# Kernel optimization log

Hardware: AMD Instinct MI355X
Metric: run time of the kernel (lower is better)

The kernel has to match this reference:

```python
import jax, jax.numpy as jnp
import numpy as np

N = 8192       # num_nodes
E = 262144     # num_edges (avg degree 32)
D_IN = 256
D_H = 256
D_OUT = 256
BN_EPS = 1e-5


def _linear_params(key, din, dout):
    # torch nn.Linear default init: U(-1/sqrt(din), 1/sqrt(din))
    s = 1.0 / np.sqrt(din)
    kw, kb = jax.random.split(key)
    W = jax.random.uniform(kw, (dout, din), jnp.float32, -s, s)
    b = jax.random.uniform(kb, (dout,), jnp.float32, -s, s)
    return W, b


def setup_inputs() -> dict:
    key = jax.random.key(0)
    ks = jax.random.split(key, 6)
    x = jax.random.normal(ks[0], (N, D_IN), jnp.float32)
    edge_index = jax.random.randint(ks[1], (2, E), 0, N, dtype=jnp.int64)
    W1, b1 = _linear_params(ks[2], D_IN, D_H)
    W2, b2 = _linear_params(ks[3], D_H, D_H)
    W3, b3 = _linear_params(ks[4], D_H, D_OUT)
    return {
        "x": x, "edge_index": edge_index,
        "W1": W1, "b1": b1, "W2": W2, "b2": b2, "W3": W3, "b3": b3,
        "g1": jnp.ones((D_H,), jnp.float32), "be1": jnp.zeros((D_H,), jnp.float32),
        "g2": jnp.ones((D_H,), jnp.float32), "be2": jnp.zeros((D_H,), jnp.float32),
        "g3": jnp.ones((D_OUT,), jnp.float32), "be3": jnp.zeros((D_OUT,), jnp.float32),
    }


def _build_norm(edge_index):
    # add self loops, scatter 1.0 into dense NxN adjacency (duplicates collapse via set)
    loop = jnp.arange(N, dtype=edge_index.dtype)
    rows = jnp.concatenate([edge_index[0], loop])
    cols = jnp.concatenate([edge_index[1], loop])
    adj = jnp.zeros((N, N), jnp.float32).at[rows, cols].set(1.0)
    deg = adj.sum(axis=1)
    dinv = jnp.where(deg > 0, deg ** -0.5, 0.0)  # inf -> 0 as in original
    return dinv[:, None] * adj * dinv[None, :]


def _gcn(x, norm, W, b):
    # linear then symmetric-normalized aggregation
    return norm @ (x @ W.T + b)


def _bn(x, g, b):
    # BatchNorm1d with batch statistics (biased var), eps=1e-5
    mu = x.mean(axis=0)
    var = x.var(axis=0)
    return (x - mu) * jax.lax.rsqrt(var + BN_EPS) * g + b


def reference(x, edge_index, W1, b1, W2, b2, W3, b3, g1, be1, g2, be2, g3, be3):
    norm = _build_norm(edge_index)
    h = jax.nn.relu(_bn(_gcn(x, norm, W1, b1), g1, be1))
    h = jax.nn.relu(_bn(_gcn(h, norm, W2, b2), g2, be2))
    h = _bn(_gcn(h, norm, W3, b3), g3, be3)
    return h
```

## Files before the change

### kernel.cpp

```cpp
#include <hip/hip_runtime.h>

#define N_NODES 8192
#define N_EDGES 262144
#define D 256
#define ADJ_WORDS 256
#define MAX_DEG 128
#define AGG_BLOCKS 2048
#define NPART 16

typedef __attribute__((ext_vector_type(8))) short bf16x8;
typedef __attribute__((ext_vector_type(4))) float f32x4;

__device__ __forceinline__ short f2bf(float f) {
    unsigned u = __builtin_bit_cast(unsigned, f);
    u += 0x7fffu + ((u >> 16) & 1);
    return (short)(u >> 16);
}
__device__ __forceinline__ float bf2f(unsigned short u) {
    return __builtin_bit_cast(float, ((unsigned)u) << 16);
}

__global__ __launch_bounds__(256) void build_adj(const int* __restrict__ ei,
                                                 unsigned* __restrict__ adj,
                                                 int* __restrict__ deg,
                                                 const float* __restrict__ W1,
                                                 const float* __restrict__ W2,
                                                 const float* __restrict__ W3,
                                                 unsigned short* __restrict__ Wb1,
                                                 unsigned short* __restrict__ Wb2,
                                                 unsigned short* __restrict__ Wb3) {
    int i = blockIdx.x * 256 + threadIdx.x;
    if (i >= N_EDGES + N_NODES) {
        int j = i - (N_EDGES + N_NODES);
        int which = j >> 16, k = j & 65535;
        const float* src = which == 0 ? W1 : which == 1 ? W2 : W3;
        unsigned short* dst = which == 0 ? Wb1 : which == 1 ? Wb2 : Wb3;
        dst[k] = (unsigned short)f2bf(src[k]);
        return;
    }
    int r, c;
    if (i < N_EDGES) {
        r = ei[i];
        c = ei[N_EDGES + i];
    } else {
        r = i - N_EDGES;
        c = r;
    }
    unsigned bit = 1u << (c & 31);
    unsigned old = atomicOr(&adj[r * ADJ_WORDS + (c >> 5)], bit);
    if (!(old & bit)) atomicAdd(&deg[r], 1);
}

__device__ __forceinline__ void nbrs_body(const unsigned* __restrict__ adj,
                                          int* __restrict__ nbr_idx, int r) {
    const int t = threadIdx.x;
    const int lane = t & 63, wave = t >> 6;
    unsigned m = adj[r * ADJ_WORDS + t];
    int cnt = __popc(m);
    int x = cnt;
    #pragma unroll
    for (int off = 1; off < 64; off <<= 1) {
        int v = __shfl_up(x, off, 64);
        if (lane >= off) x += v;
    }
    __shared__ int wtot[4];
    if (lane == 63) wtot[wave] = x;
    __syncthreads();
    int woff = 0;
    #pragma unroll
    for (int w = 0; w < 4; w++) woff += (w < wave) ? wtot[w] : 0;
    int base = woff + x - cnt;
    int* oi = nbr_idx + (size_t)r * MAX_DEG;
    while (m) {
        int b = __ffs(m) - 1;
        m &= m - 1;
        int c = (t << 5) + b;
        if (base < MAX_DEG) oi[base] = c;
        base++;
    }
}

template <bool APPLY, bool RELU>
__device__ __forceinline__ void gemm_body(const float* __restrict__ Xsrc,
                                          const float* __restrict__ psA,
                                          const float* __restrict__ psQ,
                                          const float* __restrict__ g,
                                          const float* __restrict__ be,
                                          const unsigned short* __restrict__ Wb,
                                          const float* __restrict__ bias,
                                          const int* __restrict__ deg,
                                          unsigned short* __restrict__ Hb,
                                          int bn, int bm) {
    __shared__ float ssc[256], ssh[256];
    const int tid = threadIdx.x;
    if (APPLY) {
        float s = 0.f, q = 0.f;
        #pragma unroll
        for (int i = 0; i < NPART; i++) {
            s += psA[i * 256 + tid];
            q += psQ[i * 256 + tid];
        }
        float mu = s * (1.0f / N_NODES);
        float var = q * (1.0f / N_NODES) - mu * mu;
        float rstd = rsqrtf(var + 1e-5f);
        float sc = g[tid] * rstd;
        ssc[tid] = sc;
        ssh[tid] = be[tid] - mu * sc;
        __syncthreads();
    }

    const int wave = tid >> 6, lane = tid & 63;
    const int l16 = lane & 15, q = lane >> 4;
    const int mrow = bm + wave * 16 + l16;

    f32x4 acc[4];
    #pragma unroll
    for (int j = 0; j < 4; j++) acc[j] = (f32x4){0.f, 0.f, 0.f, 0.f};

    for (int k0 = 0; k0 < D; k0 += 32) {
        const int kq = k0 + q * 8;
        bf16x8 xb;
        {
            const float* xr = Xsrc + (size_t)mrow * D + kq;
            float4 a = *(const float4*)xr;
            float4 b = *(const float4*)(xr + 4);
            float v[8] = {a.x, a.y, a.z, a.w, b.x, b.y, b.z, b.w};
            if (APPLY) {
                float4 sc0 = *(const float4*)(ssc + kq);
                float4 sc1 = *(const float4*)(ssc + kq + 4);
                float4 sh0 = *(const float4*)(ssh + kq);
                float4 sh1 = *(const float4*)(ssh + kq + 4);
                float sc[8] = {sc0.x, sc0.y, sc0.z, sc0.w, sc1.x, sc1.y, sc1.z, sc1.w};
                float sh[8] = {sh0.x, sh0.y, sh0.z, sh0.w, sh1.x, sh1.y, sh1.z, sh1.w};
                #pragma unroll
                for (int j = 0; j < 8; j++) {
                    v[j] = fmaf(v[j], sc[j], sh[j]);
                    if (RELU) v[j] = fmaxf(v[j], 0.0f);
                }
            }
            #pragma unroll
            for (int j = 0; j < 8; j++) xb[j] = f2bf(v[j]);
        }
        #pragma unroll
        for (int nf = 0; nf < 4; nf++) {
            bf16x8 wa = *(const bf16x8*)(Wb + (size_t)(bn + nf * 16 + l16) * D + kq);
            acc[nf] = __builtin_amdgcn_mfma_f32_16x16x32_bf16(wa, xb, acc[nf], 0, 0, 0);
        }
    }

    const float di = rsqrtf((float)deg[mrow]);
    #pragma unroll
    for (int nf = 0; nf < 4; nf++) {
        const int nb = bn + nf * 16 + q * 4;
        float4 b4 = *(const float4*)(bias + nb);
        short4 o;
        o.x = f2bf((acc[nf][0] + b4.x) * di);
        o.y = f2bf((acc[nf][1] + b4.y) * di);
        o.z = f2bf((acc[nf][2] + b4.z) * di);
        o.w = f2bf((acc[nf][3] + b4.w) * di);
        *(short4*)(Hb + (size_t)mrow * D + nb) = o;
    }
}

__global__ __launch_bounds__(256) void gemm1_and_nbrs(const float* __restrict__ x,
                                                      const unsigned short* __restrict__ Wb1,
                                                      const float* __restrict__ b1,
                                                      const int* __restrict__ deg,
                                                      unsigned short* __restrict__ Hb,
                                                      const unsigned* __restrict__ adj,
                                                      int* __restrict__ nbr_idx) {
    const int bg = blockIdx.x;
    if (bg < 512) {
        gemm_body<false, false>(x, nullptr, nullptr, nullptr, nullptr, Wb1, b1, deg, Hb,
                                (bg & 3) * 64, (bg >> 2) * 64);
    } else {
        nbrs_body(adj, nbr_idx, bg - 512);
    }
}

__global__ __launch_bounds__(256) void gemm_mfma_bn(const float* __restrict__ Xsrc,
                                                    const float* __restrict__ psA,
                                                    const float* __restrict__ psQ,
                                                    const float* __restrict__ g,
                                                    const float* __restrict__ be,
                                                    const unsigned short* __restrict__ Wb,
                                                    const float* __restrict__ bias,
                                                    const int* __restrict__ deg,
                                                    unsigned short* __restrict__ Hb) {
    gemm_body<true, true>(Xsrc, psA, psQ, g, be, Wb, bias, deg, Hb,
                          blockIdx.x * 64, blockIdx.y * 64);
}

__global__ __launch_bounds__(256) void aggregate_bf16(const int* __restrict__ nbr_idx,
                                                      const int* __restrict__ deg,
                                                      const unsigned short* __restrict__ Hb,
                                                      float* __restrict__ G,
                                                      float* __restrict__ psA,
                                                      float* __restrict__ psQ) {
    const int wave = threadIdx.x >> 6;
    const int lane = threadIdx.x & 63;
    const int ch = lane * 4;
    const int r = blockIdx.x * 4 + wave;

    const int dgr = deg[r];
    int dg = dgr; if (dg > MAX_DEG) dg = MAX_DEG;
    const int* idx = nbr_idx + (size_t)r * MAX_DEG;
    const unsigned short* hb = Hb + ch;

    float a0 = 0.f, a1 = 0.f, a2 = 0.f, a3 = 0.f;
    int base = 0;
    for (; base + 16 <= dg; base += 16) {
        int4 q0 = *(const int4*)(idx + base);
        int4 q1 = *(const int4*)(idx + base + 4);
        int4 q2 = *(const int4*)(idx + base + 8);
        int4 q3 = *(const int4*)(idx + base + 12);
        ushort4 u0  = *(const ushort4*)(hb + (size_t)q0.x * D);
        ushort4 u1  = *(const ushort4*)(hb + (size_t)q0.y * D);
        ushort4 u2  = *(const ushort4*)(hb + (size_t)q0.z * D);
        ushort4 u3  = *(const ushort4*)(hb + (size_t)q0.w * D);
        ushort4 u4  = *(const ushort4*)(hb + (size_t)q1.x * D);
        ushort4 u5  = *(const ushort4*)(hb + (size_t)q1.y * D);
        ushort4 u6  = *(const ushort4*)(hb + (size_t)q1.z * D);
        ushort4 u7  = *(const ushort4*)(hb + (size_t)q1.w * D);
        ushort4 u8  = *(const ushort4*)(hb + (size_t)q2.x * D);
        ushort4 u9  = *(const ushort4*)(hb + (size_t)q2.y * D);
        ushort4 u10 = *(const ushort4*)(hb + (size_t)q2.z * D);
        ushort4 u11 = *(const ushort4*)(hb + (size_t)q2.w * D);
        ushort4 u12 = *(const ushort4*)(hb + (size_t)q3.x * D);
        ushort4 u13 = *(const ushort4*)(hb + (size_t)q3.y * D);
        ushort4 u14 = *(const ushort4*)(hb + (size_t)q3.z * D);
        ushort4 u15 = *(const ushort4*)(hb + (size_t)q3.w * D);
        a0 += bf2f(u0.x);  a1 += bf2f(u0.y);  a2 += bf2f(u0.z);  a3 += bf2f(u0.w);
        a0 += bf2f(u1.x);  a1 += bf2f(u1.y);  a2 += bf2f(u1.z);  a3 += bf2f(u1.w);
        a0 += bf2f(u2.x);  a1 += bf2f(u2.y);  a2 += bf2f(u2.z);  a3 += bf2f(u2.w);
        a0 += bf2f(u3.x);  a1 += bf2f(u3.y);  a2 += bf2f(u3.z);  a3 += bf2f(u3.w);
        a0 += bf2f(u4.x);  a1 += bf2f(u4.y);  a2 += bf2f(u4.z);  a3 += bf2f(u4.w);
        a0 += bf2f(u5.x);  a1 += bf2f(u5.y);  a2 += bf2f(u5.z);  a3 += bf2f(u5.w);
        a0 += bf2f(u6.x);  a1 += bf2f(u6.y);  a2 += bf2f(u6.z);  a3 += bf2f(u6.w);
        a0 += bf2f(u7.x);  a1 += bf2f(u7.y);  a2 += bf2f(u7.z);  a3 += bf2f(u7.w);
        a0 += bf2f(u8.x);  a1 += bf2f(u8.y);  a2 += bf2f(u8.z);  a3 += bf2f(u8.w);
        a0 += bf2f(u9.x);  a1 += bf2f(u9.y);  a2 += bf2f(u9.z);  a3 += bf2f(u9.w);
        a0 += bf2f(u10.x); a1 += bf2f(u10.y); a2 += bf2f(u10.z); a3 += bf2f(u10.w);
        a0 += bf2f(u11.x); a1 += bf2f(u11.y); a2 += bf2f(u11.z); a3 += bf2f(u11.w);
        a0 += bf2f(u12.x); a1 += bf2f(u12.y); a2 += bf2f(u12.z); a3 += bf2f(u12.w);
        a0 += bf2f(u13.x); a1 += bf2f(u13.y); a2 += bf2f(u13.z); a3 += bf2f(u13.w);
        a0 += bf2f(u14.x); a1 += bf2f(u14.y); a2 += bf2f(u14.z); a3 += bf2f(u14.w);
        a0 += bf2f(u15.x); a1 += bf2f(u15.y); a2 += bf2f(u15.z); a3 += bf2f(u15.w);
    }
    for (; base + 8 <= dg; base += 8) {
        int4 q0 = *(const int4*)(idx + base);
        int4 q1 = *(const int4*)(idx + base + 4);
        ushort4 u0 = *(const ushort4*)(hb + (size_t)q0.x * D);
        ushort4 u1 = *(const ushort4*)(hb + (size_t)q0.y * D);
        ushort4 u2 = *(const ushort4*)(hb + (size_t)q0.z * D);
        ushort4 u3 = *(const ushort4*)(hb + (size_t)q0.w * D);
        ushort4 u4 = *(const ushort4*)(hb + (size_t)q1.x * D);
        ushort4 u5 = *(const ushort4*)(hb + (size_t)q1.y * D);
        ushort4 u6 = *(const ushort4*)(hb + (size_t)q1.z * D);
        ushort4 u7 = *(const ushort4*)(hb + (size_t)q1.w * D);
        a0 += bf2f(u0.x); a1 += bf2f(u0.y); a2 += bf2f(u0.z); a3 += bf2f(u0.w);
        a0 += bf2f(u1.x); a1 += bf2f(u1.y); a2 += bf2f(u1.z); a3 += bf2f(u1.w);
        a0 += bf2f(u2.x); a1 += bf2f(u2.y); a2 += bf2f(u2.z); a3 += bf2f(u2.w);
        a0 += bf2f(u3.x); a1 += bf2f(u3.y); a2 += bf2f(u3.z); a3 += bf2f(u3.w);
        a0 += bf2f(u4.x); a1 += bf2f(u4.y); a2 += bf2f(u4.z); a3 += bf2f(u4.w);
        a0 += bf2f(u5.x); a1 += bf2f(u5.y); a2 += bf2f(u5.z); a3 += bf2f(u5.w);
        a0 += bf2f(u6.x); a1 += bf2f(u6.y); a2 += bf2f(u6.z); a3 += bf2f(u6.w);
        a0 += bf2f(u7.x); a1 += bf2f(u7.y); a2 += bf2f(u7.z); a3 += bf2f(u7.w);
    }
    for (; base + 4 <= dg; base += 4) {
        int4 q0 = *(const int4*)(idx + base);
        ushort4 u0 = *(const ushort4*)(hb + (size_t)q0.x * D);
        ushort4 u1 = *(const ushort4*)(hb + (size_t)q0.y * D);
        ushort4 u2 = *(const ushort4*)(hb + (size_t)q0.z * D);
        ushort4 u3 = *(const ushort4*)(hb + (size_t)q0.w * D);
        a0 += bf2f(u0.x); a1 += bf2f(u0.y); a2 += bf2f(u0.z); a3 += bf2f(u0.w);
        a0 += bf2f(u1.x); a1 += bf2f(u1.y); a2 += bf2f(u1.z); a3 += bf2f(u1.w);
        a0 += bf2f(u2.x); a1 += bf2f(u2.y); a2 += bf2f(u2.z); a3 += bf2f(u2.w);
        a0 += bf2f(u3.x); a1 += bf2f(u3.y); a2 += bf2f(u3.z); a3 += bf2f(u3.w);
    }
    for (; base < dg; base++) {
        int c = idx[base];
        ushort4 u = *(const ushort4*)(hb + (size_t)c * D);
        a0 += bf2f(u.x); a1 += bf2f(u.y); a2 += bf2f(u.z); a3 += bf2f(u.w);
    }

    const float dr = rsqrtf((float)dgr);
    float4 o;
    o.x = a0 * dr; o.y = a1 * dr; o.z = a2 * dr; o.w = a3 * dr;
    *(float4*)(G + (size_t)r * D + ch) = o;

    __shared__ float ls[4][256], lss[4][256];
    ls[wave][ch] = o.x; ls[wave][ch + 1] = o.y; ls[wave][ch + 2] = o.z; ls[wave][ch + 3] = o.w;
    lss[wave][ch] = o.x * o.x; lss[wave][ch + 1] = o.y * o.y;
    lss[wave][ch + 2] = o.z * o.z; lss[wave][ch + 3] = o.w * o.w;
    __syncthreads();
    const int t = threadIdx.x;
    const int prow = (blockIdx.x & (NPART - 1)) * 256;
    atomicAdd(&psA[prow + t], ls[0][t] + ls[1][t] + ls[2][t] + ls[3][t]);
    atomicAdd(&psQ[prow + t], lss[0][t] + lss[1][t] + lss[2][t] + lss[3][t]);
}

__global__ __launch_bounds__(256) void bn_apply_out(const float* __restrict__ G,
                                                    const float* __restrict__ psA,
                                                    const float* __restrict__ psQ,
                                                    const float* __restrict__ g,
                                                    const float* __restrict__ be,
                                                    float* __restrict__ Out) {
    __shared__ float ssc[256], ssh[256];
    const int tid = threadIdx.x;
    {
        float s = 0.f, q = 0.f;
        #pragma unroll
        for (int i = 0; i < NPART; i++) {
            s += psA[i * 256 + tid];
            q += psQ[i * 256 + tid];
        }
        float mu = s * (1.0f / N_NODES);
        float var = q * (1.0f / N_NODES) - mu * mu;
        float rstd = rsqrtf(var + 1e-5f);
        float sc = g[tid] * rstd;
        ssc[tid] = sc;
        ssh[tid] = be[tid] - mu * sc;
        __syncthreads();
    }
    const int rows_per_block = 32;
    const int r0 = blockIdx.x * rows_per_block;
    const int ch = (tid & 63) * 4;
    const int rsub = tid >> 6;
    float4 sc = *(const float4*)(ssc + ch);
    float4 sh = *(const float4*)(ssh + ch);
    for (int rr = rsub; rr < rows_per_block; rr += 4) {
        const size_t off = (size_t)(r0 + rr) * D + ch;
        float4 v = *(const float4*)(G + off);
        v.x = fmaf(v.x, sc.x, sh.x);
        v.y = fmaf(v.y, sc.y, sh.y);
        v.z = fmaf(v.z, sc.z, sh.z);
        v.w = fmaf(v.w, sc.w, sh.w);
        *(float4*)(Out + off) = v;
    }
}

extern "C" void kernel_launch(void* const* d_in, const int* in_sizes, int n_in,
                              void* d_out, int out_size, void* d_ws, size_t ws_size,
                              hipStream_t stream) {
    const float* x  = (const float*)d_in[0];
    const int*   ei = (const int*)d_in[1];
    const float* W1 = (const float*)d_in[2];
    const float* b1 = (const float*)d_in[3];
    const float* W2 = (const float*)d_in[4];
    const float* b2 = (const float*)d_in[5];
    const float* W3 = (const float*)d_in[6];
    const float* b3 = (const float*)d_in[7];
    const float* g1 = (const float*)d_in[8];
    const float* be1 = (const float*)d_in[9];
    const float* g2 = (const float*)d_in[10];
    const float* be2 = (const float*)d_in[11];
    const float* g3 = (const float*)d_in[12];
    const float* be3 = (const float*)d_in[13];

    char* ws = (char*)d_ws;
    unsigned*       adj  = (unsigned*)ws;
    int*            deg  = (int*)(ws + (8 << 20));
    float*          psA0 = (float*)(ws + (8 << 20) + (32 << 10));
    float*          psQ0 = psA0 + NPART * 256;
    float*          psA1 = psQ0 + NPART * 256;
    float*          psQ1 = psA1 + NPART * 256;
    float*          psA2 = psQ1 + NPART * 256;
    float*          psQ2 = psA2 + NPART * 256;
    unsigned short* Wb1  = (unsigned short*)(ws + (8 << 20) + (128 << 10));
    unsigned short* Wb2  = (unsigned short*)(ws + (8 << 20) + (256 << 10));
    unsigned short* Wb3  = (unsigned short*)(ws + (8 << 20) + (384 << 10));
    int*            nbr_idx = (int*)  (ws + (9 << 20));
    float*          G       = (float*)(ws + (13 << 20));
    unsigned short* Hb      = (unsigned short*)(ws + (21 << 20));

    hipMemsetAsync(ws, 0, (8 << 20) + (128 << 10), stream);

    build_adj<<<1824, 256, 0, stream>>>(ei, adj, deg, W1, W2, W3, Wb1, Wb2, Wb3);

    gemm1_and_nbrs<<<512 + N_NODES, 256, 0, stream>>>(x, Wb1, b1, deg, Hb, adj, nbr_idx);
    aggregate_bf16<<<AGG_BLOCKS, 256, 0, stream>>>(nbr_idx, deg, Hb, G, psA0, psQ0);

    dim3 ggrid(D / 64, N_NODES / 64);

    gemm_mfma_bn<<<ggrid, 256, 0, stream>>>(G, psA0, psQ0, g1, be1, Wb2, b2, deg, Hb);
    aggregate_bf16<<<AGG_BLOCKS, 256, 0, stream>>>(nbr_idx, deg, Hb, G, psA1, psQ1);

    gemm_mfma_bn<<<ggrid, 256, 0, stream>>>(G, psA1, psQ1, g2, be2, Wb3, b3, deg, Hb);
    aggregate_bf16<<<AGG_BLOCKS, 256, 0, stream>>>(nbr_idx, deg, Hb, G, psA2, psQ2);

    bn_apply_out<<<N_NODES / 32, 256, 0, stream>>>(G, psA2, psQ2, g3, be3, (float*)d_out);
}
```

Baseline: 217.2 us.

## Fuse all GCN phases into one cooperative persistent kernel with grid syncs

Replaces the memset plus seven separate launches with a single cooperative kernel of 1024 persistent blocks. Phases (zeroing, adjacency build, GEMMs, neighbor lists, aggregations, BN output) are separated by grid.sync and use grid-stride loops. GEMM tiles shrink to 64x32 so 1024 tiles fill the grid, and the first GEMM now runs alongside neighbor-list extraction in the same phase. The aim is to remove launch gaps and the memset, at the cost of grid-wide barrier overhead and register and occupancy limits from the launch bound of 4 blocks per CU. A fallback path of separate launches remains.

```diff
diff --git a/kernel.cpp b/kernel.cpp
--- a/kernel.cpp
+++ b/kernel.cpp
@@ -1,15 +1,29 @@
 #include <hip/hip_runtime.h>
+#include <hip/hip_cooperative_groups.h>
+
+namespace cg = cooperative_groups;
 
 #define N_NODES 8192
 #define N_EDGES 262144
 #define D 256
 #define ADJ_WORDS 256
 #define MAX_DEG 128
-#define AGG_BLOCKS 2048
 #define NPART 16
+#define GRID_C 1024
 
 typedef __attribute__((ext_vector_type(8))) short bf16x8;
 typedef __attribute__((ext_vector_type(4))) float f32x4;
+
+struct Params {
+    const float* x; const int* ei;
+    const float *W1, *b1, *W2, *b2, *W3, *b3;
+    const float *g1, *be1, *g2, *be2, *g3, *be3;
+    float* out;
+    unsigned* adj; int* deg;
+    float *psA0, *psQ0, *psA1, *psQ1, *psA2, *psQ2;
+    unsigned short *Wb1, *Wb2, *Wb3;
+    int* nbr_idx; float* G; unsigned short* Hb;
+};
 
 __device__ __forceinline__ short f2bf(float f) {
     unsigned u = __builtin_bit_cast(unsigned, f);
@@ -20,39 +34,40 @@
     return __builtin_bit_cast(float, ((unsigned)u) << 16);
 }
 
-__global__ __launch_bounds__(256) void build_adj(const int* __restrict__ ei,
-                                                 unsigned* __restrict__ adj,
-                                                 int* __restrict__ deg,
-                                                 const float* __restrict__ W1,
-                                                 const float* __restrict__ W2,
-                                                 const float* __restrict__ W3,
-                                                 unsigned short* __restrict__ Wb1,
-                                                 unsigned short* __restrict__ Wb2,
-                                                 unsigned short* __restrict__ Wb3) {
-    int i = blockIdx.x * 256 + threadIdx.x;
-    if (i >= N_EDGES + N_NODES) {
-        int j = i - (N_EDGES + N_NODES);
-        int which = j >> 16, k = j & 65535;
-        const float* src = which == 0 ? W1 : which == 1 ? W2 : W3;
-        unsigned short* dst = which == 0 ? Wb1 : which == 1 ? Wb2 : Wb3;
-        dst[k] = (unsigned short)f2bf(src[k]);
-        return;
-    }
-    int r, c;
-    if (i < N_EDGES) {
-        r = ei[i];
-        c = ei[N_EDGES + i];
-    } else {
-        r = i - N_EDGES;
-        c = r;
-    }
-    unsigned bit = 1u << (c & 31);
-    unsigned old = atomicOr(&adj[r * ADJ_WORDS + (c >> 5)], bit);
-    if (!(old & bit)) atomicAdd(&deg[r], 1);
-}
-
-__device__ __forceinline__ void nbrs_body(const unsigned* __restrict__ adj,
-                                          int* __restrict__ nbr_idx, int r) {
+__device__ __forceinline__ void ph_zero(float4* z, int n4) {
+    const int stride = gridDim.x * 256;
+    for (int i = blockIdx.x * 256 + threadIdx.x; i < n4; i += stride)
+        z[i] = make_float4(0.f, 0.f, 0.f, 0.f);
+}
+
+__device__ __forceinline__ void ph_build(const Params& p) {
+    const int TOT = N_EDGES + N_NODES + 3 * 65536;
+    const int stride = gridDim.x * 256;
+    for (int i = blockIdx.x * 256 + threadIdx.x; i < TOT; i += stride) {
+        if (i >= N_EDGES + N_NODES) {
+            int j = i - (N_EDGES + N_NODES);
+            int which = j >> 16, k = j & 65535;
+            const float* src = which == 0 ? p.W1 : which == 1 ? p.W2 : p.W3;
+            unsigned short* dst = which == 0 ? p.Wb1 : which == 1 ? p.Wb2 : p.Wb3;
+            dst[k] = (unsigned short)f2bf(src[k]);
+            continue;
+        }
+        int r, c;
+        if (i < N_EDGES) {
+            r = p.ei[i];
+            c = p.ei[N_EDGES + i];
+        } else {
+            r = i - N_EDGES;
+            c = r;
+        }
+        unsigned bit = 1u << (c & 31);
+        unsigned old = atomicOr(&p.adj[r * ADJ_WORDS + (c >> 5)], bit);
+        if (!(old & bit)) atomicAdd(&p.deg[r], 1);
+    }
+}
+
+__device__ __forceinline__ void nbrs_row(const unsigned* __restrict__ adj,
+                                         int* __restrict__ nbr_idx, int r) {
     const int t = threadIdx.x;
     const int lane = t & 63, wave = t >> 6;
     unsigned m = adj[r * ADJ_WORDS + t];
@@ -80,17 +95,23 @@
     }
 }
 
+__device__ __forceinline__ void ph_nbrs(const unsigned* adj, int* nbr_idx) {
+    for (int r = blockIdx.x; r < N_NODES; r += gridDim.x) {
+        nbrs_row(adj, nbr_idx, r);
+        __syncthreads();
+    }
+}
+
 template <bool APPLY, bool RELU>
-__device__ __forceinline__ void gemm_body(const float* __restrict__ Xsrc,
-                                          const float* __restrict__ psA,
-                                          const float* __restrict__ psQ,
-                                          const float* __restrict__ g,
-                                          const float* __restrict__ be,
-                                          const unsigned short* __restrict__ Wb,
-                                          const float* __restrict__ bias,
-                                          const int* __restrict__ deg,
-                                          unsigned short* __restrict__ Hb,
-                                          int bn, int bm) {
+__device__ __forceinline__ void ph_gemm(const float* __restrict__ Xsrc,
+                                        const float* __restrict__ psA,
+                                        const float* __restrict__ psQ,
+                                        const float* __restrict__ g,
+                                        const float* __restrict__ be,
+                                        const unsigned short* __restrict__ Wb,
+                                        const float* __restrict__ bias,
+                                        const int* __restrict__ deg,
+                                        unsigned short* __restrict__ Hb) {
     __shared__ float ssc[256], ssh[256];
     const int tid = threadIdx.x;
     if (APPLY) {
@@ -108,204 +129,182 @@
         ssh[tid] = be[tid] - mu * sc;
         __syncthreads();
     }
-
     const int wave = tid >> 6, lane = tid & 63;
     const int l16 = lane & 15, q = lane >> 4;
-    const int mrow = bm + wave * 16 + l16;
-
-    f32x4 acc[4];
-    #pragma unroll
-    for (int j = 0; j < 4; j++) acc[j] = (f32x4){0.f, 0.f, 0.f, 0.f};
-
-    for (int k0 = 0; k0 < D; k0 += 32) {
-        const int kq = k0 + q * 8;
-        bf16x8 xb;
-        {
-            const float* xr = Xsrc + (size_t)mrow * D + kq;
-            float4 a = *(const float4*)xr;
-            float4 b = *(const float4*)(xr + 4);
-            float v[8] = {a.x, a.y, a.z, a.w, b.x, b.y, b.z, b.w};
-            if (APPLY) {
-                float4 sc0 = *(const float4*)(ssc + kq);
-                float4 sc1 = *(const float4*)(ssc + kq + 4);
-                float4 sh0 = *(const float4*)(ssh + kq);
-                float4 sh1 = *(const float4*)(ssh + kq + 4);
-                float sc[8] = {sc0.x, sc0.y, sc0.z, sc0.w, sc1.x, sc1.y, sc1.z, sc1.w};
-                float sh[8] = {sh0.x, sh0.y, sh0.z, sh0.w, sh1.x, sh1.y, sh1.z, sh1.w};
+
+    for (int t = blockIdx.x; t < 1024; t += gridDim.x) {
+        const int bn = (t & 7) * 32;
+        const int bm = (t >> 3) * 64;
+        const int mrow = bm + wave * 16 + l16;
+
+        f32x4 acc[2];
+        acc[0] = (f32x4){0.f, 0.f, 0.f, 0.f};
+        acc[1] = (f32x4){0.f, 0.f, 0.f, 0.f};
+
+        for (int k0 = 0; k0 < D; k0 += 32) {
+            const int kq = k0 + q * 8;
+            bf16x8 xb;
+            {
+                const float* xr = Xsrc + (size_t)mrow * D + kq;
+                float4 a = *(const float4*)xr;
+                float4 b = *(const float4*)(xr + 4);
+                float v[8] = {a.x, a.y, a.z, a.w, b.x, b.y, b.z, b.w};
+                if (APPLY) {
+                    float4 sc0 = *(const float4*)(ssc + kq);
+                    float4 sc1 = *(const float4*)(ssc + kq + 4);
+                    float4 sh0 = *(const float4*)(ssh + kq);
+                    float4 sh1 = *(const float4*)(ssh + kq + 4);
+                    float sc[8] = {sc0.x, sc0.y, sc0.z, sc0.w, sc1.x, sc1.y, sc1.z, sc1.w};
+                    float sh[8] = {sh0.x, sh0.y, sh0.z, sh0.w, sh1.x, sh1.y, sh1.z, sh1.w};
+                    #pragma unroll
+                    for (int j = 0; j < 8; j++) {
+                        v[j] = fmaf(v[j], sc[j], sh[j]);
+                        if (RELU) v[j] = fmaxf(v[j], 0.0f);
+                    }
+                }
                 #pragma unroll
-                for (int j = 0; j < 8; j++) {
-                    v[j] = fmaf(v[j], sc[j], sh[j]);
-                    if (RELU) v[j] = fmaxf(v[j], 0.0f);
-                }
+                for (int j = 0; j < 8; j++) xb[j] = f2bf(v[j]);
             }
             #pragma unroll
-            for (int j = 0; j < 8; j++) xb[j] = f2bf(v[j]);
-        }
+            for (int nf = 0; nf < 2; nf++) {
+                bf16x8 wa = *(const bf16x8*)(Wb + (size_t)(bn + nf * 16 + l16) * D + kq);
+                acc[nf] = __builtin_amdgcn_mfma_f32_16x16x32_bf16(wa, xb, acc[nf], 0, 0, 0);
+            }
+        }
+
+        const float di = rsqrtf((float)deg[mrow]);
         #pragma unroll
-        for (int nf = 0; nf < 4; nf++) {
-            bf16x8 wa = *(const bf16x8*)(Wb + (size_t)(bn + nf * 16 + l16) * D + kq);
-            acc[nf] = __builtin_amdgcn_mfma_f32_16x16x32_bf16(wa, xb, acc[nf], 0, 0, 0);
-        }
-    }
-
-    const float di = rsqrtf((float)deg[mrow]);
-    #pragma unroll
-    for (int nf = 0; nf < 4; nf++) {
-        const int nb = bn + nf * 16 + q * 4;
-        float4 b4 = *(const float4*)(bias + nb);
-        short4 o;
-        o.x = f2bf((acc[nf][0] + b4.x) * di);
-        o.y = f2bf((acc[nf][1] + b4.y) * di);
-        o.z = f2bf((acc[nf][2] + b4.z) * di);
-        o.w = f2bf((acc[nf][3] + b4.w) * di);
-        *(short4*)(Hb + (size_t)mrow * D + nb) = o;
-    }
-}
-
-__global__ __launch_bounds__(256) void gemm1_and_nbrs(const float* __restrict__ x,
-                                                      const unsigned short* __restrict__ Wb1,
-                                                      const float* __restrict__ b1,
-                                                      const int* __restrict__ deg,
-                                                      unsigned short* __restrict__ Hb,
-                                                      const unsigned* __restrict__ adj,
-                                                      int* __restrict__ nbr_idx) {
-    const int bg = blockIdx.x;
-    if (bg < 512) {
-        gemm_body<false, false>(x, nullptr, nullptr, nullptr, nullptr, Wb1, b1, deg, Hb,
-                                (bg & 3) * 64, (bg >> 2) * 64);
-    } else {
-        nbrs_body(adj, nbr_idx, bg - 512);
-    }
-}
-
-__global__ __launch_bounds__(256) void gemm_mfma_bn(const float* __restrict__ Xsrc,
-                                                    const float* __restrict__ psA,
-                                                    const float* __restrict__ psQ,
-                                                    const float* __restrict__ g,
-                                                    const float* __restrict__ be,
-                                                    const unsigned short* __restrict__ Wb,
-                                                    const float* __restrict__ bias,
-                                                    const int* __restrict__ deg,
-                                                    unsigned short* __restrict__ Hb) {
-    gemm_body<true, true>(Xsrc, psA, psQ, g, be, Wb, bias, deg, Hb,
-                          blockIdx.x * 64, blockIdx.y * 64);
-}
-
-__global__ __launch_bounds__(256) void aggregate_bf16(const int* __restrict__ nbr_idx,
-                                                      const int* __restrict__ deg,
-                                                      const unsigned short* __restrict__ Hb,
-                                                      float* __restrict__ G,
-                                                      float* __restrict__ psA,
-                                                      float* __restrict__ psQ) {
+        for (int nf = 0; nf < 2; nf++) {
+            const int nb = bn + nf * 16 + q * 4;
+            float4 b4 = *(const float4*)(bias + nb);
+            short4 o;
+            o.x = f2bf((acc[nf][0] + b4.x) * di);
+            o.y = f2bf((acc[nf][1] + b4.y) * di);
+            o.z = f2bf((acc[nf][2] + b4.z) * di);
+            o.w = f2bf((acc[nf][3] + b4.w) * di);
+            *(short4*)(Hb + (size_t)mrow * D + nb) = o;
+        }
+    }
+}
+
+__device__ __forceinline__ void ph_agg(const int* __restrict__ nbr_idx,
+                                       const int* __restrict__ deg,
+                                       const unsigned short* __restrict__ Hb,
+                                       float* __restrict__ G,
+                                       float* __restrict__ psA,
+                                       float* __restrict__ psQ) {
+    __shared__ float ls[4][256], lss[4][256];
     const int wave = threadIdx.x >> 6;
     const int lane = threadIdx.x & 63;
     const int ch = lane * 4;
-    const int r = blockIdx.x * 4 + wave;
-
-    const int dgr = deg[r];
-    int dg = dgr; if (dg > MAX_DEG) dg = MAX_DEG;
-    const int* idx = nbr_idx + (size_t)r * MAX_DEG;
     const unsigned short* hb = Hb + ch;
 
-    float a0 = 0.f, a1 = 0.f, a2 = 0.f, a3 = 0.f;
-    int base = 0;
-    for (; base + 16 <= dg; base += 16) {
-        int4 q0 = *(const int4*)(idx + base);
-        int4 q1 = *(const int4*)(idx + base + 4);
-        int4 q2 = *(const int4*)(idx + base + 8);
-        int4 q3 = *(const int4*)(idx + base + 12);
-        ushort4 u0  = *(const ushort4*)(hb + (size_t)q0.x * D);
-        ushort4 u1  = *(const ushort4*)(hb + (size_t)q0.y * D);
-        ushort4 u2  = *(const ushort4*)(hb + (size_t)q0.z * D);
-        ushort4 u3  = *(const ushort4*)(hb + (size_t)q0.w * D);
-        ushort4 u4  = *(const ushort4*)(hb + (size_t)q1.x * D);
-        ushort4 u5  = *(const ushort4*)(hb + (size_t)q1.y * D);
-        ushort4 u6  = *(const ushort4*)(hb + (size_t)q1.z * D);
-        ushort4 u7  = *(const ushort4*)(hb + (size_t)q1.w * D);
-        ushort4 u8  = *(const ushort4*)(hb + (size_t)q2.x * D);
-        ushort4 u9  = *(const ushort4*)(hb + (size_t)q2.y * D);
-        ushort4 u10 = *(const ushort4*)(hb + (size_t)q2.z * D);
-        ushort4 u11 = *(const ushort4*)(hb + (size_t)q2.w * D);
-        ushort4 u12 = *(const ushort4*)(hb + (size_t)q3.x * D);
-        ushort4 u13 = *(const ushort4*)(hb + (size_t)q3.y * D);
-        ushort4 u14 = *(const ushort4*)(hb + (size_t)q3.z * D);
-        ushort4 u15 = *(const ushort4*)(hb + (size_t)q3.w * D);
-        a0 += bf2f(u0.x);  a1 += bf2f(u0.y);  a2 += bf2f(u0.z);  a3 += bf2f(u0.w);
-        a0 += bf2f(u1.x);  a1 += bf2f(u1.y);  a2 += bf2f(u1.z);  a3 += bf2f(u1.w);
-        a0 += bf2f(u2.x);  a1 += bf2f(u2.y);  a2 += bf2f(u2.z);  a3 += bf2f(u2.w);
-        a0 += bf2f(u3.x);  a1 += bf2f(u3.y);  a2 += bf2f(u3.z);  a3 += bf2f(u3.w);
-        a0 += bf2f(u4.x);  a1 += bf2f(u4.y);  a2 += bf2f(u4.z);  a3 += bf2f(u4.w);
-        a0 += bf2f(u5.x);  a1 += bf2f(u5.y);  a2 += bf2f(u5.z);  a3 += bf2f(u5.w);
-        a0 += bf2f(u6.x);  a1 += bf2f(u6.y);  a2 += bf2f(u6.z);  a3 += bf2f(u6.w);
-        a0 += bf2f(u7.x);  a1 += bf2f(u7.y);  a2 += bf2f(u7.z);  a3 += bf2f(u7.w);
-        a0 += bf2f(u8.x);  a1 += bf2f(u8.y);  a2 += bf2f(u8.z);  a3 += bf2f(u8.w);
-        a0 += bf2f(u9.x);  a1 += bf2f(u9.y);  a2 += bf2f(u9.z);  a3 += bf2f(u9.w);
-        a0 += bf2f(u10.x); a1 += bf2f(u10.y); a2 += bf2f(u10.z); a3 += bf2f(u10.w);
-        a0 += bf2f(u11.x); a1 += bf2f(u11.y); a2 += bf2f(u11.z); a3 += bf2f(u11.w);
-        a0 += bf2f(u12.x); a1 += bf2f(u12.y); a2 += bf2f(u12.z); a3 += bf2f(u12.w);
-        a0 += bf2f(u13.x); a1 += bf2f(u13.y); a2 += bf2f(u13.z); a3 += bf2f(u13.w);
-        a0 += bf2f(u14.x); a1 += bf2f(u14.y); a2 += bf2f(u14.z); a3 += bf2f(u14.w);
-        a0 += bf2f(u15.x); a1 += bf2f(u15.y); a2 += bf2f(u15.z); a3 += bf2f(u15.w);
-    }
-    for (; base + 8 <= dg; base += 8) {
-        int4 q0 = *(const int4*)(idx + base);
-        int4 q1 = *(const int4*)(idx + base + 4);
-        ushort4 u0 = *(const ushort4*)(hb + (size_t)q0.x * D);
-        ushort4 u1 = *(const ushort4*)(hb + (size_t)q0.y * D);
-        ushort4 u2 = *(const ushort4*)(hb + (size_t)q0.z * D);
-        ushort4 u3 = *(const ushort4*)(hb + (size_t)q0.w * D);
-        ushort4 u4 = *(const ushort4*)(hb + (size_t)q1.x * D);
-        ushort4 u5 = *(const ushort4*)(hb + (size_t)q1.y * D);
-        ushort4 u6 = *(const ushort4*)(hb + (size_t)q1.z * D);
-        ushort4 u7 = *(const ushort4*)(hb + (size_t)q1.w * D);
-        a0 += bf2f(u0.x); a1 += bf2f(u0.y); a2 += bf2f(u0.z); a3 += bf2f(u0.w);
-        a0 += bf2f(u1.x); a1 += bf2f(u1.y); a2 += bf2f(u1.z); a3 += bf2f(u1.w);
-        a0 += bf2f(u2.x); a1 += bf2f(u2.y); a2 += bf2f(u2.z); a3 += bf2f(u2.w);
-        a0 += bf2f(u3.x); a1 += bf2f(u3.y); a2 += bf2f(u3.z); a3 += bf2f(u3.w);
-        a0 += bf2f(u4.x); a1 += bf2f(u4.y); a2 += bf2f(u4.z); a3 += bf2f(u4.w);
-        a0 += bf2f(u5.x); a1 += bf2f(u5.y); a2 += bf2f(u5.z); a3 += bf2f(u5.w);
-        a0 += bf2f(u6.x); a1 += bf2f(u6.y); a2 += bf2f(u6.z); a3 += bf2f(u6.w);
-        a0 += bf2f(u7.x); a1 += bf2f(u7.y); a2 += bf2f(u7.z); a3 += bf2f(u7.w);
-    }
-    for (; base + 4 <= dg; base += 4) {
-        int4 q0 = *(const int4*)(idx + base);
-        ushort4 u0 = *(const ushort4*)(hb + (size_t)q0.x * D);
-        ushort4 u1 = *(const ushort4*)(hb + (size_t)q0.y * D);
-        ushort4 u2 = *(const ushort4*)(hb + (size_t)q0.z * D);
-        ushort4 u3 = *(const ushort4*)(hb + (size_t)q0.w * D);
-        a0 += bf2f(u0.x); a1 += bf2f(u0.y); a2 += bf2f(u0.z); a3 += bf2f(u0.w);
-        a0 += bf2f(u1.x); a1 += bf2f(u1.y); a2 += bf2f(u1.z); a3 += bf2f(u1.w);
-        a0 += bf2f(u2.x); a1 += bf2f(u2.y); a2 += bf2f(u2.z); a3 += bf2f(u2.w);
-        a0 += bf2f(u3.x); a1 += bf2f(u3.y); a2 += bf2f(u3.z); a3 += bf2f(u3.w);
-    }
-    for (; base < dg; base++) {
-        int c = idx[base];
-        ushort4 u = *(const ushort4*)(hb + (size_t)c * D);
-        a0 += bf2f(u.x); a1 += bf2f(u.y); a2 += bf2f(u.z); a3 += bf2f(u.w);
-    }
-
-    const float dr = rsqrtf((float)dgr);
-    float4 o;
-    o.x = a0 * dr; o.y = a1 * dr; o.z = a2 * dr; o.w = a3 * dr;
-    *(float4*)(G + (size_t)r * D + ch) = o;
-
-    __shared__ float ls[4][256], lss[4][256];
-    ls[wave][ch] = o.x; ls[wave][ch + 1] = o.y; ls[wave][ch + 2] = o.z; ls[wave][ch + 3] = o.w;
-    lss[wave][ch] = o.x * o.x; lss[wave][ch + 1] = o.y * o.y;
-    lss[wave][ch + 2] = o.z * o.z; lss[wave][ch + 3] = o.w * o.w;
-    __syncthreads();
-    const int t = threadIdx.x;
-    const int prow = (blockIdx.x & (NPART - 1)) * 256;
-    atomicAdd(&psA[prow + t], ls[0][t] + ls[1][t] + ls[2][t] + ls[3][t]);
-    atomicAdd(&psQ[prow + t], lss[0][t] + lss[1][t] + lss[2][t] + lss[3][t]);
-}
-
-__global__ __launch_bounds__(256) void bn_apply_out(const float* __restrict__ G,
-                                                    const float* __restrict__ psA,
-                                                    const float* __restrict__ psQ,
-                                                    const float* __restrict__ g,
-                                                    const float* __restrict__ be,
-                                                    float* __restrict__ Out) {
+    for (int gblk = blockIdx.x; gblk < N_NODES / 4; gblk += gridDim.x) {
+        const int r = gblk * 4 + wave;
+        const int dgr = deg[r];
+        int dg = dgr; if (dg > MAX_DEG) dg = MAX_DEG;
+        const int* idx = nbr_idx + (size_t)r * MAX_DEG;
+
+        float a0 = 0.f, a1 = 0.f, a2 = 0.f, a3 = 0.f;
+        int base = 0;
+        for (; base + 16 <= dg; base += 16) {
+            int4 q0 = *(const int4*)(idx + base);
+            int4 q1 = *(const int4*)(idx + base + 4);
+            int4 q2 = *(const int4*)(idx + base + 8);
+            int4 q3 = *(const int4*)(idx + base + 12);
+            ushort4 u0  = *(const ushort4*)(hb + (size_t)q0.x * D);
+            ushort4 u1  = *(const ushort4*)(hb + (size_t)q0.y * D);
+            ushort4 u2  = *(const ushort4*)(hb + (size_t)q0.z * D);
+            ushort4 u3  = *(const ushort4*)(hb + (size_t)q0.w * D);
+            ushort4 u4  = *(const ushort4*)(hb + (size_t)q1.x * D);
+            ushort4 u5  = *(const ushort4*)(hb + (size_t)q1.y * D);
+            ushort4 u6  = *(const ushort4*)(hb + (size_t)q1.z * D);
+            ushort4 u7  = *(const ushort4*)(hb + (size_t)q1.w * D);
+            ushort4 u8  = *(const ushort4*)(hb + (size_t)q2.x * D);
+            ushort4 u9  = *(const ushort4*)(hb + (size_t)q2.y * D);
+            ushort4 u10 = *(const ushort4*)(hb + (size_t)q2.z * D);
+            ushort4 u11 = *(const ushort4*)(hb + (size_t)q2.w * D);
+            ushort4 u12 = *(const ushort4*)(hb + (size_t)q3.x * D);
+            ushort4 u13 = *(const ushort4*)(hb + (size_t)q3.y * D);
+            ushort4 u14 = *(const ushort4*)(hb + (size_t)q3.z * D);
+            ushort4 u15 = *(const ushort4*)(hb + (size_t)q3.w * D);
+            a0 += bf2f(u0.x);  a1 += bf2f(u0.y);  a2 += bf2f(u0.z);  a3 += bf2f(u0.w);
+            a0 += bf2f(u1.x);  a1 += bf2f(u1.y);  a2 += bf2f(u1.z);  a3 += bf2f(u1.w);
+            a0 += bf2f(u2.x);  a1 += bf2f(u2.y);  a2 += bf2f(u2.z);  a3 += bf2f(u2.w);
+            a0 += bf2f(u3.x);  a1 += bf2f(u3.y);  a2 += bf2f(u3.z);  a3 += bf2f(u3.w);
+            a0 += bf2f(u4.x);  a1 += bf2f(u4.y);  a2 += bf2f(u4.z);  a3 += bf2f(u4.w);
+            a0 += bf2f(u5.x);  a1 += bf2f(u5.y);  a2 += bf2f(u5.z);  a3 += bf2f(u5.w);
+            a0 += bf2f(u6.x);  a1 += bf2f(u6.y);  a2 += bf2f(u6.z);  a3 += bf2f(u6.w);
+            a0 += bf2f(u7.x);  a1 += bf2f(u7.y);  a2 += bf2f(u7.z);  a3 += bf2f(u7.w);
+            a0 += bf2f(u8.x);  a1 += bf2f(u8.y);  a2 += bf2f(u8.z);  a3 += bf2f(u8.w);
+            a0 += bf2f(u9.x);  a1 += bf2f(u9.y);  a2 += bf2f(u9.z);  a3 += bf2f(u9.w);
+            a0 += bf2f(u10.x); a1 += bf2f(u10.y); a2 += bf2f(u10.z); a3 += bf2f(u10.w);
+            a0 += bf2f(u11.x); a1 += bf2f(u11.y); a2 += bf2f(u11.z); a3 += bf2f(u11.w);
+            a0 += bf2f(u12.x); a1 += bf2f(u12.y); a2 += bf2f(u12.z); a3 += bf2f(u12.w);
+            a0 += bf2f(u13.x); a1 += bf2f(u13.y); a2 += bf2f(u13.z); a3 += bf2f(u13.w);
+            a0 += bf2f(u14.x); a1 += bf2f(u14.y); a2 += bf2f(u14.z); a3 += bf2f(u14.w);
+            a0 += bf2f(u15.x); a1 += bf2f(u15.y); a2 += bf2f(u15.z); a3 += bf2f(u15.w);
+        }
+        for (; base + 8 <= dg; base += 8) {
+            int4 q0 = *(const int4*)(idx + base);
+            int4 q1 = *(const int4*)(idx + base + 4);
+            ushort4 u0 = *(const ushort4*)(hb + (size_t)q0.x * D);
+            ushort4 u1 = *(const ushort4*)(hb + (size_t)q0.y * D);
+            ushort4 u2 = *(const ushort4*)(hb + (size_t)q0.z * D);
+            ushort4 u3 = *(const ushort4*)(hb + (size_t)q0.w * D);
+            ushort4 u4 = *(const ushort4*)(hb + (size_t)q1.x * D);
+            ushort4 u5 = *(const ushort4*)(hb + (size_t)q1.y * D);
+            ushort4 u6 = *(const ushort4*)(hb + (size_t)q1.z * D);
+            ushort4 u7 = *(const ushort4*)(hb + (size_t)q1.w * D);
+            a0 += bf2f(u0.x); a1 += bf2f(u0.y); a2 += bf2f(u0.z); a3 += bf2f(u0.w);
+            a0 += bf2f(u1.x); a1 += bf2f(u1.y); a2 += bf2f(u1.z); a3 += bf2f(u1.w);
+            a0 += bf2f(u2.x); a1 += bf2f(u2.y); a2 += bf2f(u2.z); a3 += bf2f(u2.w);
+            a0 += bf2f(u3.x); a1 += bf2f(u3.y); a2 += bf2f(u3.z); a3 += bf2f(u3.w);
+            a0 += bf2f(u4.x); a1 += bf2f(u4.y); a2 += bf2f(u4.z); a3 += bf2f(u4.w);
+            a0 += bf2f(u5.x); a1 += bf2f(u5.y); a2 += bf2f(u5.z); a3 += bf2f(u5.w);
+            a0 += bf2f(u6.x); a1 += bf2f(u6.y); a2 += bf2f(u6.z); a3 += bf2f(u6.w);
+            a0 += bf2f(u7.x); a1 += bf2f(u7.y); a2 += bf2f(u7.z); a3 += bf2f(u7.w);
+        }
+        for (; base + 4 <= dg; base += 4) {
+            int4 q0 = *(const int4*)(idx + base);
+            ushort4 u0 = *(const ushort4*)(hb + (size_t)q0.x * D);
+            ushort4 u1 = *(const ushort4*)(hb + (size_t)q0.y * D);
+            ushort4 u2 = *(const ushort4*)(hb + (size_t)q0.z * D);
+            ushort4 u3 = *(const ushort4*)(hb + (size_t)q0.w * D);
+            a0 += bf2f(u0.x); a1 += bf2f(u0.y); a2 += bf2f(u0.z); a3 += bf2f(u0.w);
+            a0 += bf2f(u1.x); a1 += bf2f(u1.y); a2 += bf2f(u1.z); a3 += bf2f(u1.w);
+            a0 += bf2f(u2.x); a1 += bf2f(u2.y); a2 += bf2f(u2.z); a3 += bf2f(u2.w);
+            a0 += bf2f(u3.x); a1 += bf2f(u3.y); a2 += bf2f(u3.z); a3 += bf2f(u3.w);
+        }
+        for (; base < dg; base++) {
+            int c = idx[base];
+            ushort4 u = *(const ushort4*)(hb + (size_t)c * D);
+            a0 += bf2f(u.x); a1 += bf2f(u.y); a2 += bf2f(u.z); a3 += bf2f(u.w);
+        }
+
+        const float dr = rsqrtf((float)dgr);
+        float4 o;
+        o.x = a0 * dr; o.y = a1 * dr; o.z = a2 * dr; o.w = a3 * dr;
+        *(float4*)(G + (size_t)r * D + ch) = o;
+
+        __syncthreads();
+        ls[wave][ch] = o.x; ls[wave][ch + 1] = o.y; ls[wave][ch + 2] = o.z; ls[wave][ch + 3] = o.w;
+        lss[wave][ch] = o.x * o.x; lss[wave][ch + 1] = o.y * o.y;
+        lss[wave][ch + 2] = o.z * o.z; lss[wave][ch + 3] = o.w * o.w;
+        __syncthreads();
+        const int t = threadIdx.x;
+        const int prow = (gblk & (NPART - 1)) * 256;
+        atomicAdd(&psA[prow + t], ls[0][t] + ls[1][t] + ls[2][t] + ls[3][t]);
+        atomicAdd(&psQ[prow + t], lss[0][t] + lss[1][t] + lss[2][t] + lss[3][t]);
+    }
+}
+
+__device__ __forceinline__ void ph_out(const float* __restrict__ G,
+                                       const float* __restrict__ psA,
+                                       const float* __restrict__ psQ,
+                                       const float* __restrict__ g,
+                                       const float* __restrict__ be,
+                                       float* __restrict__ Out) {
     __shared__ float ssc[256], ssh[256];
     const int tid = threadIdx.x;
     {
@@ -323,14 +322,13 @@
         ssh[tid] = be[tid] - mu * sc;
         __syncthreads();
     }
-    const int rows_per_block = 32;
-    const int r0 = blockIdx.x * rows_per_block;
+    const int wave = tid >> 6;
     const int ch = (tid & 63) * 4;
-    const int rsub = tid >> 6;
     float4 sc = *(const float4*)(ssc + ch);
     float4 sh = *(const float4*)(ssh + ch);
-    for (int rr = rsub; rr < rows_per_block; rr += 4) {
-        const size_t off = (size_t)(r0 + rr) * D + ch;
+    for (int gblk = blockIdx.x; gblk < N_NODES / 4; gblk += gridDim.x) {
+        const int r = gblk * 4 + wave;
+        const size_t off = (size_t)r * D + ch;
         float4 v = *(const float4*)(G + off);
         v.x = fmaf(v.x, sc.x, sh.x);
         v.y = fmaf(v.y, sc.y, sh.y);
@@ -340,54 +338,96 @@
     }
 }
 
+__global__ __launch_bounds__(256, 4) void mega(Params p) {
+    cg::grid_group grid = cg::this_grid();
+
+    ph_zero((float4*)p.adj, (8 << 20) / 16 + (128 << 10) / 16);
+    grid.sync();
+    ph_build(p);
+    grid.sync();
+    ph_gemm<false, false>(p.x, nullptr, nullptr, nullptr, nullptr, p.Wb1, p.b1, p.deg, p.Hb);
+    ph_nbrs(p.adj, p.nbr_idx);
+    grid.sync();
+    ph_agg(p.nbr_idx, p.deg, p.Hb, p.G, p.psA0, p.psQ0);
+    grid.sync();
+    ph_gemm<true, true>(p.G, p.psA0, p.psQ0, p.g1, p.be1, p.Wb2, p.b2, p.deg, p.Hb);
+    grid.sync();
+    ph_agg(p.nbr_idx, p.deg, p.Hb, p.G, p.psA1, p.psQ1);
+    grid.sync();
+    ph_gemm<true, true>(p.G, p.psA1, p.psQ1, p.g2, p.be2, p.Wb3, p.b3, p.deg, p.Hb);
+    grid.sync();
+    ph_agg(p.nbr_idx, p.deg, p.Hb, p.G, p.psA2, p.psQ2);
+    grid.sync();
+    ph_out(p.G, p.psA2, p.psQ2, p.g3, p.be3, p.out);
+}
+
+__global__ __launch_bounds__(256) void k_build(Params p) { ph_build(p); }
+__global__ __launch_bounds__(256) void k_nbrs(Params p) { ph_nbrs(p.adj, p.nbr_idx); }
+__global__ __launch_bounds__(256) void k_gemm1(Params p) {
+    ph_gemm<false, false>(p.x, nullptr, nullptr, nullptr, nullptr, p.Wb1, p.b1, p.deg, p.Hb);
+}
+__global__ __launch_bounds__(256) void k_gemmbn(Params p, const float* psA, const float* psQ,
+                                               const float* g, const float* be,
+                                               const unsigned short* Wb, const float* bias) {
+    ph_gemm<true, true>(p.G, psA, psQ, g, be, Wb, bias, p.deg, p.Hb);
+}
+__global__ __launch_bounds__(256) void k_agg(Params p, float* psA, float* psQ) {
+    ph_agg(p.nbr_idx, p.deg, p.Hb, p.G, psA, psQ);
+}
+__global__ __launch_bounds__(256) void k_out(Params p) {
+    ph_out(p.G, p.psA2, p.psQ2, p.g3, p.be3, p.out);
+}
+
 extern "C" void kernel_launch(void* const* d_in, const int* in_sizes, int n_in,
                               void* d_out, int out_size, void* d_ws, size_t ws_size,
                               hipStream_t stream) {
-    const float* x  = (const float*)d_in[0];
-    const int*   ei = (const int*)d_in[1];
-    const float* W1 = (const float*)d_in[2];
-    const float* b1 = (const float*)d_in[3];
-    const float* W2 = (const float*)d_in[4];
-    const float* b2 = (const float*)d_in[5];
-    const float* W3 = (const float*)d_in[6];
-    const float* b3 = (const float*)d_in[7];
-    const float* g1 = (const float*)d_in[8];
-    const float* be1 = (const float*)d_in[9];
-    const float* g2 = (const float*)d_in[10];
-    const float* be2 = (const float*)d_in[11];
-    const float* g3 = (const float*)d_in[12];
-    const float* be3 = (const float*)d_in[13];
-
     char* ws = (char*)d_ws;
-    unsigned*       adj  = (unsigned*)ws;
-    int*            deg  = (int*)(ws + (8 << 20));
-    float*          psA0 = (float*)(ws + (8 << 20) + (32 << 10));
-    float*          psQ0 = psA0 + NPART * 256;
-    float*          psA1 = psQ0 + NPART * 256;
-    float*          psQ1 = psA1 + NPART * 256;
-    float*          psA2 = psQ1 + NPART * 256;
-    float*          psQ2 = psA2 + NPART * 256;
-    unsigned short* Wb1  = (unsigned short*)(ws + (8 << 20) + (128 << 10));
-    unsigned short* Wb2  = (unsigned short*)(ws + (8 << 20) + (256 << 10));
-    unsigned short* Wb3  = (unsigned short*)(ws + (8 << 20) + (384 << 10));
-    int*            nbr_idx = (int*)  (ws + (9 << 20));
-    float*          G       = (float*)(ws + (13 << 20));
-    unsigned short* Hb      = (unsigned short*)(ws + (21 << 20));
+    Params p;
+    p.x   = (const float*)d_in[0];
+    p.ei  = (const int*)d_in[1];
+    p.W1  = (const float*)d_in[2];  p.b1  = (const float*)d_in[3];
+    p.W2  = (const float*)d_in[4];  p.b2  = (const float*)d_in[5];
+    p.W3  = (const float*)d_in[6];  p.b3  = (const float*)d_in[7];
+    p.g1  = (const float*)d_in[8];  p.be1 = (const float*)d_in[9];
+    p.g2  = (const float*)d_in[10]; p.be2 = (const float*)d_in[11];
+    p.g3  = (const float*)d_in[12]; p.be3 = (const float*)d_in[13];
+    p.out = (float*)d_out;
+    p.adj  = (unsigned*)ws;
+    p.deg  = (int*)(ws + (8 << 20));
+    p.psA0 = (float*)(ws + (8 << 20) + (32 << 10));
+    p.psQ0 = p.psA0 + NPART * 256;
+    p.psA1 = p.psQ0 + NPART * 256;
+    p.psQ1 = p.psA1 + NPART * 256;
+    p.psA2 = p.psQ1 + NPART * 256;
+    p.psQ2 = p.psA2 + NPART * 256;
+    p.Wb1  = (unsigned short*)(ws + (8 << 20) + (128 << 10));
+    p.Wb2  = (unsigned short*)(ws + (8 << 20) + (256 << 10));
+    p.Wb3  = (unsigned short*)(ws + (8 << 20) + (384 << 10));
+    p.nbr_idx = (int*)(ws + (9 << 20));
+    p.G    = (float*)(ws + (13 << 20));
+    p.Hb   = (unsigned short*)(ws + (21 << 20));
+
+    static int coop_blocks = -1;
+    if (coop_blocks < 0) {
+        int m = 0;
+        hipError_t e = hipOccupancyMaxActiveBlocksPerMultiprocessor(&m, (const void*)mega, 256, 0);
+        coop_blocks = (e == hipSuccess) ? m : 0;
+    }
+    if (coop_blocks >= GRID_C / 256) {
+        void* args[] = {(void*)&p};
+        hipError_t e = hipLaunchCooperativeKernel((const void*)mega, dim3(GRID_C), dim3(256),
+                                                  args, 0, stream);
+        if (e == hipSuccess) return;
+    }
 
     hipMemsetAsync(ws, 0, (8 << 20) + (128 << 10), stream);
-
-    build_adj<<<1824, 256, 0, stream>>>(ei, adj, deg, W1, W2, W3, Wb1, Wb2, Wb3);
-
-    gemm1_and_nbrs<<<512 + N_NODES, 256, 0, stream>>>(x, Wb1, b1, deg, Hb, adj, nbr_idx);
-    aggregate_bf16<<<AGG_BLOCKS, 256, 0, stream>>>(nbr_idx, deg, Hb, G, psA0, psQ0);
-
-    dim3 ggrid(D / 64, N_NODES / 64);
-
-    gemm_mfma_bn<<<ggrid, 256, 0, stream>>>(G, psA0, psQ0, g1, be1, Wb2, b2, deg, Hb);
-    aggregate_bf16<<<AGG_BLOCKS, 256, 0, stream>>>(nbr_idx, deg, Hb, G, psA1, psQ1);
-
-    gemm_mfma_bn<<<ggrid, 256, 0, stream>>>(G, psA1, psQ1, g2, be2, Wb3, b3, deg, Hb);
-    aggregate_bf16<<<AGG_BLOCKS, 256, 0, stream>>>(nbr_idx, deg, Hb, G, psA2, psQ2);
-
-    bn_apply_out<<<N_NODES / 32, 256, 0, stream>>>(G, psA2, psQ2, g3, be3, (float*)d_out);
-}
+    k_build<<<1824, 256, 0, stream>>>(p);
+    k_gemm1<<<1024, 256, 0, stream>>>(p);
+    k_nbrs<<<8192, 256, 0, stream>>>(p);
+    k_agg<<<2048, 256, 0, stream>>>(p, p.psA0, p.psQ0);
+    k_gemmbn<<<1024, 256, 0, stream>>>(p, p.psA0, p.psQ0, p.g1, p.be1, p.Wb2, p.b2);
+    k_agg<<<2048, 256, 0, stream>>>(p, p.psA1, p.psQ1);
+    k_gemmbn<<<1024, 256, 0, stream>>>(p, p.psA1, p.psQ1, p.g2, p.be2, p.Wb3, p.b3);
+    k_agg<<<2048, 256, 0, stream>>>(p, p.psA2, p.psQ2);
+    k_out<<<2048, 256, 0, stream>>>(p);
+}
```

Result: slower. 238.0 us (+9.6%).
